# Kernel optimization log

Hardware: AMD Instinct MI355X
Metric: run time of the kernel (lower is better)

The kernel has to match this reference:

```python
import jax, jax.numpy as jnp
import numpy as np

IN_C = 1
BASE_C = 16
N3, N2, N1 = 262144, 65536, 16384

def _quadconv(feat, neigh, w, b):
    # feat: [N, C]; neigh: [N, 9] with -1 padding -> gather via extra zero row
    N = feat.shape[0]
    feat_p = jnp.concatenate([feat, jnp.zeros((1, feat.shape[1]), feat.dtype)], axis=0)
    gidx = jnp.where(neigh == -1, N, neigh)
    col = feat_p[gidx].reshape(N, -1)  # [N, 9*C] im2col
    return col @ w.T + b

def _parent_idx(keys, parent_keys):
    return jnp.searchsorted(parent_keys, keys >> 2)

def _quadpool(feat, keys, parent_keys):
    pidx = _parent_idx(keys, parent_keys)
    p = jax.ops.segment_max(feat, pidx, num_segments=parent_keys.shape[0])
    # original inits with -1e9 and zeroes untouched slots; segment_max uses -inf fill
    return jnp.where(jnp.isneginf(p), jnp.zeros((), feat.dtype), p), pidx

def _quadunpool(feat, keys, parent_keys):
    return feat[_parent_idx(keys, parent_keys)]

def _lin(key, out_f, in_f, scale=0.05):
    kw, kb = jax.random.split(key)
    return (jax.random.normal(kw, (out_f, in_f), jnp.float32) * scale,
            jnp.zeros((out_f,), jnp.float32))

def setup_inputs() -> dict:
    key = jax.random.key(0)
    ks = jax.random.split(key, 12)
    inp = {
        'features': jax.random.normal(ks[0], (N3, IN_C), jnp.float32),
        'keys3': jnp.arange(N3, dtype=jnp.int32),
        'keys2': jnp.arange(N2, dtype=jnp.int32),
        'keys1': jnp.arange(N1, dtype=jnp.int32),
        'neighs3': jax.random.randint(ks[1], (N3, 9), -1, N3, jnp.int32),
        'neighs2': jax.random.randint(ks[2], (N2, 9), -1, N2, jnp.int32),
        'neighs1': jax.random.randint(ks[3], (N1, 9), -1, N1, jnp.int32),
    }
    c = BASE_C
    inp['w_enc1'], inp['b_enc1'] = _lin(ks[4], c, 9 * IN_C)
    inp['w_enc2'], inp['b_enc2'] = _lin(ks[5], 2 * c, 9 * c)
    inp['w_enc3'], inp['b_enc3'] = _lin(ks[6], 4 * c, 9 * 2 * c)
    inp['w_dec1'], inp['b_dec1'] = _lin(ks[7], 2 * c, 9 * 4 * c)
    inp['w_dec2'], inp['b_dec2'] = _lin(ks[8], c, 9 * 2 * c)
    inp['w_head'], inp['b_head'] = _lin(ks[9], IN_C, 9 * c)
    return inp

def reference(features, keys3, keys2, keys1, neighs3, neighs2, neighs1,
              w_enc1, b_enc1, w_enc2, b_enc2, w_enc3, b_enc3,
              w_dec1, b_dec1, w_dec2, b_dec2, w_head, b_head):
    relu = jax.nn.relu
    x8 = relu(_quadconv(features, neighs3, w_enc1, b_enc1))
    x7_p, _ = _quadpool(x8, keys3, keys2)
    x7 = relu(_quadconv(x7_p, neighs2, w_enc2, b_enc2))
    x6_p, _ = _quadpool(x7, keys2, keys1)
    x6 = relu(_quadconv(x6_p, neighs1, w_enc3, b_enc3))
    x7_up = _quadunpool(x6, keys2, keys1)
    x7_dec = relu(_quadconv(x7_up, neighs2, w_dec1, b_dec1))
    x8_up = _quadunpool(x7_dec, keys3, keys2)
    x8_dec = relu(_quadconv(x8_up, neighs3, w_dec2, b_dec2))
    return _quadconv(x8_dec, neighs3, w_head, b_head)
```

## Files before the change

kernel.cpp:

```cpp
#include <hip/hip_runtime.h>
#include <stdint.h>

#define NN3 262144
#define NN2 65536
#define NN1 16384

typedef __attribute__((ext_vector_type(8))) __bf16 bf16x8;
typedef __attribute__((ext_vector_type(4))) float floatx4;

static __device__ __forceinline__ float bf2f(unsigned short u) {
    union { unsigned int i; float f; } v; v.i = ((unsigned int)u) << 16; return v.f;
}
static __device__ __forceinline__ unsigned short f2bf(float f) {
    union { float f; unsigned int i; } v; v.f = f;
    unsigned int x = v.i;
    return (unsigned short)((x + 0x7fffu + ((x >> 16) & 1u)) >> 16);
}
static __device__ __forceinline__ bf16x8 zero_bf16x8() {
    bf16x8 z;
#pragma unroll
    for (int i = 0; i < 8; ++i) z[i] = (__bf16)0.0f;
    return z;
}

__global__ __launch_bounds__(256) void enc1pool_kernel(
    const float* __restrict__ feat, const int* __restrict__ neigh,
    const float* __restrict__ w, const float* __restrict__ b,
    unsigned short* __restrict__ x7p,
    const float* __restrict__ w_enc2, const float* __restrict__ w_enc3,
    const float* __restrict__ w_dec1, const float* __restrict__ w_dec2,
    unsigned short* __restrict__ wb_enc2, unsigned short* __restrict__ wb_enc3,
    unsigned short* __restrict__ wb_dec1, unsigned short* __restrict__ wb_dec2)
{
    {
        int g = blockIdx.x * 256 + threadIdx.x;
        if (g < 4608) wb_enc2[g] = f2bf(w_enc2[g]);
        else {
            g -= 4608;
            if (g < 18432) wb_enc3[g] = f2bf(w_enc3[g]);
            else {
                g -= 18432;
                if (g < 18432) wb_dec1[g] = f2bf(w_dec1[g]);
                else { g -= 18432; if (g < 4608) wb_dec2[g] = f2bf(w_dec2[g]); }
            }
        }
    }
    __shared__ float ws[144];
    __shared__ float bs[16];
    __shared__ int nsh[2304];
    int t = threadIdx.x;
    if (t < 144) ws[t] = w[t];
    if (t < 16)  bs[t] = b[t];
    int base = blockIdx.x * 256;
    for (int e = t; e < 2304; e += 256)
        nsh[e] = __builtin_nontemporal_load(&neigh[(size_t)base * 9 + e]);
    __syncthreads();
    float f[9];
#pragma unroll
    for (int k = 0; k < 9; ++k) { int j = nsh[t * 9 + k]; f[k] = (j < 0) ? 0.0f : feat[j]; }
    float v[16];
#pragma unroll
    for (int co = 0; co < 16; ++co) {
        float a = bs[co];
#pragma unroll
        for (int k = 0; k < 9; ++k) a += f[k] * ws[co * 9 + k];
        v[co] = fmaxf(a, 0.0f);
    }
#pragma unroll
    for (int co = 0; co < 16; ++co) {
        v[co] = fmaxf(v[co], __shfl_xor(v[co], 1));
        v[co] = fmaxf(v[co], __shfl_xor(v[co], 2));
    }
    if ((t & 3) == 0) {
        unsigned int ov[8];
#pragma unroll
        for (int h = 0; h < 8; ++h)
            ov[h] = (unsigned int)f2bf(v[2 * h]) | (((unsigned int)f2bf(v[2 * h + 1])) << 16);
        uint4* dst = (uint4*)(x7p + (size_t)((base + t) >> 2) * 16);
        dst[0] = make_uint4(ov[0], ov[1], ov[2], ov[3]);
        dst[1] = make_uint4(ov[4], ov[5], ov[6], ov[7]);
    }
}

template <int CIN, int COUT, bool SHIFT, bool POOL, int TILES>
__global__ __launch_bounds__(256) void conv_mfma(
    const unsigned short* __restrict__ src, const int* __restrict__ neigh,
    const unsigned short* __restrict__ wb, const float* __restrict__ bias,
    unsigned short* __restrict__ dst)
{
    constexpr int K  = 9 * CIN;
    constexpr int KT = (K + 31) / 32;
    constexpr int NT = COUT / 16;
    __shared__ int nsh[576 * TILES];
    int t = threadIdx.x;
    int rowbase = blockIdx.x * (64 * TILES);
    for (int e = t; e < 576 * TILES; e += 256) {
        int j = __builtin_nontemporal_load(&neigh[(size_t)rowbase * 9 + e]);
        if (SHIFT) j = (j < 0) ? -1 : (j >> 2);
        nsh[e] = j;
    }
    __syncthreads();
    int lane = t & 63;
    int wave = t >> 6;
    int m    = lane & 15;
    int quad = lane >> 4;
    int mrow9 = (wave * 16 + m) * 9;
    floatx4 acc[TILES][NT];
#pragma unroll
    for (int tl = 0; tl < TILES; ++tl)
#pragma unroll
        for (int n = 0; n < NT; ++n) acc[tl][n] = (floatx4){0.f, 0.f, 0.f, 0.f};
    for (int kt = 0; kt < KT; ++kt) {
        int k0 = kt * 32 + quad * 8;
        bf16x8 a[TILES];
#pragma unroll
        for (int tl = 0; tl < TILES; ++tl) {
            a[tl] = zero_bf16x8();
            if (k0 < K) {
                int nb = k0 / CIN;
                int ci = k0 % CIN;
                int j  = nsh[tl * 576 + mrow9 + nb];
                if (j >= 0) a[tl] = *(const bf16x8*)(src + (size_t)j * CIN + ci);
            }
        }
#pragma unroll
        for (int n = 0; n < NT; ++n) {
            bf16x8 bfrag = zero_bf16x8();
            if (k0 < K) bfrag = *(const bf16x8*)(wb + (size_t)(n * 16 + m) * K + k0);
#pragma unroll
            for (int tl = 0; tl < TILES; ++tl)
                acc[tl][n] = __builtin_amdgcn_mfma_f32_16x16x32_bf16(a[tl], bfrag, acc[tl][n], 0, 0, 0);
        }
    }
#pragma unroll
    for (int tl = 0; tl < TILES; ++tl) {
        int tbase = rowbase + tl * 64;
        if (POOL) {
            int p = (tbase >> 2) + wave * 4 + quad;
#pragma unroll
            for (int n = 0; n < NT; ++n) {
                int cout = n * 16 + m;
                float vm = fmaxf(fmaxf(acc[tl][n][0], acc[tl][n][1]), fmaxf(acc[tl][n][2], acc[tl][n][3]));
                float v  = fmaxf(vm + bias[cout], 0.0f);
                dst[(size_t)p * COUT + cout] = f2bf(v);
            }
        } else {
            int grow = tbase + wave * 16 + quad * 4;
#pragma unroll
            for (int n = 0; n < NT; ++n) {
                int cout = n * 16 + m;
                float bv = bias[cout];
#pragma unroll
                for (int r = 0; r < 4; ++r) {
                    float v = fmaxf(acc[tl][n][r] + bv, 0.0f);
                    dst[(size_t)(grow + r) * COUT + cout] = f2bf(v);
                }
            }
        }
    }
}

static __device__ __forceinline__ float dot2(unsigned int u, const float* w) {
    return bf2f((unsigned short)(u & 0xffffu)) * w[0] + bf2f((unsigned short)(u >> 16)) * w[1];
}
__global__ __launch_bounds__(256) void head_kernel(
    const unsigned short* __restrict__ x, const int* __restrict__ neigh,
    const float* __restrict__ w, const float* __restrict__ b, float* __restrict__ out)
{
    __shared__ float ws[144];
    __shared__ int nsh[4608];
    int t = threadIdx.x;
    if (t < 144) ws[t] = w[t];
    int base = blockIdx.x * 512;
    for (int e = t; e < 4608; e += 256)
        nsh[e] = __builtin_nontemporal_load(&neigh[(size_t)base * 9 + e]);
    __syncthreads();
    float acc0 = b[0], acc1 = b[0];
#pragma unroll
    for (int k = 0; k < 9; ++k) {
        int j0 = nsh[t * 9 + k];
        int j1 = nsh[(256 + t) * 9 + k];
        const float* wp = &ws[k * 16];
        if (j0 >= 0) {
            const uint4* r = (const uint4*)(x + (size_t)j0 * 16);
            uint4 r0 = r[0], r1 = r[1];
            acc0 += dot2(r0.x, wp)     + dot2(r0.y, wp + 2)  + dot2(r0.z, wp + 4)  + dot2(r0.w, wp + 6);
            acc0 += dot2(r1.x, wp + 8) + dot2(r1.y, wp + 10) + dot2(r1.z, wp + 12) + dot2(r1.w, wp + 14);
        }
        if (j1 >= 0) {
            const uint4* r = (const uint4*)(x + (size_t)j1 * 16);
            uint4 r0 = r[0], r1 = r[1];
            acc1 += dot2(r0.x, wp)     + dot2(r0.y, wp + 2)  + dot2(r0.z, wp + 4)  + dot2(r0.w, wp + 6);
            acc1 += dot2(r1.x, wp + 8) + dot2(r1.y, wp + 10) + dot2(r1.z, wp + 12) + dot2(r1.w, wp + 14);
        }
    }
    __builtin_nontemporal_store(acc0, &out[base + t]);
    __builtin_nontemporal_store(acc1, &out[base + 256 + t]);
}

extern "C" void kernel_launch(void* const* d_in, const int* in_sizes, int n_in,
                              void* d_out, int out_size, void* d_ws, size_t ws_size,
                              hipStream_t stream) {
    const float* features = (const float*)d_in[0];
    const int* neighs3 = (const int*)d_in[4];
    const int* neighs2 = (const int*)d_in[5];
    const int* neighs1 = (const int*)d_in[6];
    const float* w_enc1 = (const float*)d_in[7];
    const float* b_enc1 = (const float*)d_in[8];
    const float* w_enc2 = (const float*)d_in[9];
    const float* b_enc2 = (const float*)d_in[10];
    const float* w_enc3 = (const float*)d_in[11];
    const float* b_enc3 = (const float*)d_in[12];
    const float* w_dec1 = (const float*)d_in[13];
    const float* b_dec1 = (const float*)d_in[14];
    const float* w_dec2 = (const float*)d_in[15];
    const float* b_dec2 = (const float*)d_in[16];
    const float* w_head = (const float*)d_in[17];
    const float* b_head = (const float*)d_in[18];

    char* ws = (char*)d_ws;
    size_t off = 0;
    unsigned short* wb_enc2 = (unsigned short*)(ws + off); off += 4608 * 2;
    unsigned short* wb_enc3 = (unsigned short*)(ws + off); off += 18432 * 2;
    unsigned short* wb_dec1 = (unsigned short*)(ws + off); off += 18432 * 2;
    unsigned short* wb_dec2 = (unsigned short*)(ws + off); off += 4608 * 2;
    unsigned short* x7p   = (unsigned short*)(ws + off); off += (size_t)NN2 * 16 * 2;
    unsigned short* x6p   = (unsigned short*)(ws + off); off += (size_t)NN1 * 32 * 2;
    unsigned short* x6    = (unsigned short*)(ws + off); off += (size_t)NN1 * 64 * 2;
    unsigned short* x7dec = (unsigned short*)(ws + off); off += (size_t)NN2 * 32 * 2;
    unsigned short* x8dec = (unsigned short*)(ws + off); off += (size_t)NN3 * 16 * 2;

    enc1pool_kernel<<<NN3 / 256, 256, 0, stream>>>(features, neighs3, w_enc1, b_enc1, x7p,
                                                   w_enc2, w_enc3, w_dec1, w_dec2,
                                                   wb_enc2, wb_enc3, wb_dec1, wb_dec2);
    conv_mfma<16, 32, false, true, 2><<<NN2 / 128, 256, 0, stream>>>(x7p, neighs2, wb_enc2, b_enc2, x6p);
    conv_mfma<32, 64, false, false, 1><<<NN1 / 64, 256, 0, stream>>>(x6p, neighs1, wb_enc3, b_enc3, x6);
    conv_mfma<64, 32, true, false, 2><<<NN2 / 128, 256, 0, stream>>>(x6, neighs2, wb_dec1, b_dec1, x7dec);
    conv_mfma<32, 16, true, false, 4><<<NN3 / 256, 256, 0, stream>>>(x7dec, neighs3, wb_dec2, b_dec2, x8dec);
    head_kernel<<<NN3 / 512, 256, 0, stream>>>(x8dec, neighs3, w_head, b_head, (float*)d_out);
}
```

Baseline: 204.3 us.

## Split conv waves across output columns, pre-swizzle weights, prefetch gathers

Weights are pre-swizzled into MFMA fragment order, zero-padded along K, so each lane loads its B fragment with one contiguous, coalesced read and no bounds check. Waves are now split along output channels (WN) as well as rows, so blocks cover fewer rows and the grid gets more blocks for the small middle layers. The A-operand neighbor gather for the next K step is issued before the current MFMAs to hide gather latency. The trade-offs are more register pressure from the double-buffered fragments and fully unrolled K loop, and repeated A gathers across the waves that share rows.

```diff
diff --git a/kernel.cpp b/kernel.cpp
--- a/kernel.cpp
+++ b/kernel.cpp
@@ -21,6 +21,21 @@
 #pragma unroll
     for (int i = 0; i < 8; ++i) z[i] = (__bf16)0.0f;
     return z;
+}
+
+template <int CIN, int COUT>
+static __device__ __forceinline__ void prep_swz(const float* __restrict__ w,
+                                                unsigned short* __restrict__ out, int g) {
+    constexpr int K = 9 * CIN, KT = (K + 31) / 32;
+    int n = g / (KT * 512);
+    int r = g - n * (KT * 512);
+    int kt = r >> 9;
+    int q = r & 511;
+    int lane = q >> 3, e = q & 7;
+    int m = lane & 15, quad = lane >> 4;
+    int k = kt * 32 + quad * 8 + e;
+    float v = (k < K) ? w[(n * 16 + m) * K + k] : 0.0f;
+    out[g] = f2bf(v);
 }
 
 __global__ __launch_bounds__(256) void enc1pool_kernel(
@@ -34,14 +49,14 @@
 {
     {
         int g = blockIdx.x * 256 + threadIdx.x;
-        if (g < 4608) wb_enc2[g] = f2bf(w_enc2[g]);
+        if (g < 5120) prep_swz<16, 32>(w_enc2, wb_enc2, g);
         else {
-            g -= 4608;
-            if (g < 18432) wb_enc3[g] = f2bf(w_enc3[g]);
+            g -= 5120;
+            if (g < 18432) prep_swz<32, 64>(w_enc3, wb_enc3, g);
             else {
                 g -= 18432;
-                if (g < 18432) wb_dec1[g] = f2bf(w_dec1[g]);
-                else { g -= 18432; if (g < 4608) wb_dec2[g] = f2bf(w_dec2[g]); }
+                if (g < 18432) prep_swz<64, 32>(w_dec1, wb_dec1, g);
+                else { g -= 18432; if (g < 4608) prep_swz<32, 16>(w_dec2, wb_dec2, g); }
             }
         }
     }
@@ -82,19 +97,22 @@
     }
 }
 
-template <int CIN, int COUT, bool SHIFT, bool POOL, int TILES>
+template <int CIN, int COUT, bool SHIFT, bool POOL, int TILES, int WN>
 __global__ __launch_bounds__(256) void conv_mfma(
     const unsigned short* __restrict__ src, const int* __restrict__ neigh,
     const unsigned short* __restrict__ wb, const float* __restrict__ bias,
     unsigned short* __restrict__ dst)
 {
-    constexpr int K  = 9 * CIN;
-    constexpr int KT = (K + 31) / 32;
-    constexpr int NT = COUT / 16;
-    __shared__ int nsh[576 * TILES];
+    constexpr int K   = 9 * CIN;
+    constexpr int KT  = (K + 31) / 32;
+    constexpr int NT  = COUT / 16;
+    constexpr int WM  = 4 / WN;
+    constexpr int NTW = NT / WN;
+    constexpr int ROWS = WM * TILES * 16;
+    __shared__ int nsh[ROWS * 9];
     int t = threadIdx.x;
-    int rowbase = blockIdx.x * (64 * TILES);
-    for (int e = t; e < 576 * TILES; e += 256) {
+    int rowbase = blockIdx.x * ROWS;
+    for (int e = t; e < ROWS * 9; e += 256) {
         int j = __builtin_nontemporal_load(&neigh[(size_t)rowbase * 9 + e]);
         if (SHIFT) j = (j < 0) ? -1 : (j >> 2);
         nsh[e] = j;
@@ -102,53 +120,67 @@
     __syncthreads();
     int lane = t & 63;
     int wave = t >> 6;
+    int wm   = wave / WN;
+    int wn   = wave - wm * WN;
     int m    = lane & 15;
     int quad = lane >> 4;
-    int mrow9 = (wave * 16 + m) * 9;
-    floatx4 acc[TILES][NT];
+    int rbase9[TILES];
 #pragma unroll
     for (int tl = 0; tl < TILES; ++tl)
-#pragma unroll
-        for (int n = 0; n < NT; ++n) acc[tl][n] = (floatx4){0.f, 0.f, 0.f, 0.f};
+        rbase9[tl] = ((wm * TILES + tl) * 16 + m) * 9;
+
+    floatx4 acc[TILES][NTW];
+#pragma unroll
+    for (int tl = 0; tl < TILES; ++tl)
+#pragma unroll
+        for (int n = 0; n < NTW; ++n) acc[tl][n] = (floatx4){0.f, 0.f, 0.f, 0.f};
+
+    auto gatherA = [&](int kt, bf16x8 (&dstA)[TILES]) {
+        int k0 = kt * 32 + quad * 8;
+#pragma unroll
+        for (int tl = 0; tl < TILES; ++tl) {
+            dstA[tl] = zero_bf16x8();
+            if (k0 < K) {
+                int j = nsh[rbase9[tl] + k0 / CIN];
+                if (j >= 0) dstA[tl] = *(const bf16x8*)(src + (size_t)j * CIN + (k0 % CIN));
+            }
+        }
+    };
+
+    bf16x8 aC[TILES], aP[TILES];
+    gatherA(0, aC);
+#pragma unroll
     for (int kt = 0; kt < KT; ++kt) {
-        int k0 = kt * 32 + quad * 8;
-        bf16x8 a[TILES];
-#pragma unroll
-        for (int tl = 0; tl < TILES; ++tl) {
-            a[tl] = zero_bf16x8();
-            if (k0 < K) {
-                int nb = k0 / CIN;
-                int ci = k0 % CIN;
-                int j  = nsh[tl * 576 + mrow9 + nb];
-                if (j >= 0) a[tl] = *(const bf16x8*)(src + (size_t)j * CIN + ci);
-            }
-        }
-#pragma unroll
-        for (int n = 0; n < NT; ++n) {
-            bf16x8 bfrag = zero_bf16x8();
-            if (k0 < K) bfrag = *(const bf16x8*)(wb + (size_t)(n * 16 + m) * K + k0);
+        if (kt + 1 < KT) gatherA(kt + 1, aP);
+#pragma unroll
+        for (int n = 0; n < NTW; ++n) {
+            int ng = wn * NTW + n;
+            bf16x8 bfrag = *(const bf16x8*)(wb + ((size_t)(ng * KT + kt) * 64 + lane) * 8);
 #pragma unroll
             for (int tl = 0; tl < TILES; ++tl)
-                acc[tl][n] = __builtin_amdgcn_mfma_f32_16x16x32_bf16(a[tl], bfrag, acc[tl][n], 0, 0, 0);
-        }
-    }
+                acc[tl][n] = __builtin_amdgcn_mfma_f32_16x16x32_bf16(aC[tl], bfrag, acc[tl][n], 0, 0, 0);
+        }
+#pragma unroll
+        for (int tl = 0; tl < TILES; ++tl) aC[tl] = aP[tl];
+    }
+
 #pragma unroll
     for (int tl = 0; tl < TILES; ++tl) {
-        int tbase = rowbase + tl * 64;
+        int rg = wm * TILES + tl;
         if (POOL) {
-            int p = (tbase >> 2) + wave * 4 + quad;
-#pragma unroll
-            for (int n = 0; n < NT; ++n) {
-                int cout = n * 16 + m;
+            int p = (rowbase >> 2) + rg * 4 + quad;
+#pragma unroll
+            for (int n = 0; n < NTW; ++n) {
+                int cout = (wn * NTW + n) * 16 + m;
                 float vm = fmaxf(fmaxf(acc[tl][n][0], acc[tl][n][1]), fmaxf(acc[tl][n][2], acc[tl][n][3]));
                 float v  = fmaxf(vm + bias[cout], 0.0f);
                 dst[(size_t)p * COUT + cout] = f2bf(v);
             }
         } else {
-            int grow = tbase + wave * 16 + quad * 4;
-#pragma unroll
-            for (int n = 0; n < NT; ++n) {
-                int cout = n * 16 + m;
+            int grow = rowbase + rg * 16 + quad * 4;
+#pragma unroll
+            for (int n = 0; n < NTW; ++n) {
+                int cout = (wn * NTW + n) * 16 + m;
                 float bv = bias[cout];
 #pragma unroll
                 for (int r = 0; r < 4; ++r) {
@@ -220,7 +252,7 @@
 
     char* ws = (char*)d_ws;
     size_t off = 0;
-    unsigned short* wb_enc2 = (unsigned short*)(ws + off); off += 4608 * 2;
+    unsigned short* wb_enc2 = (unsigned short*)(ws + off); off += 5120 * 2;
     unsigned short* wb_enc3 = (unsigned short*)(ws + off); off += 18432 * 2;
     unsigned short* wb_dec1 = (unsigned short*)(ws + off); off += 18432 * 2;
     unsigned short* wb_dec2 = (unsigned short*)(ws + off); off += 4608 * 2;
@@ -233,9 +265,9 @@
     enc1pool_kernel<<<NN3 / 256, 256, 0, stream>>>(features, neighs3, w_enc1, b_enc1, x7p,
                                                    w_enc2, w_enc3, w_dec1, w_dec2,
                                                    wb_enc2, wb_enc3, wb_dec1, wb_dec2);
-    conv_mfma<16, 32, false, true, 2><<<NN2 / 128, 256, 0, stream>>>(x7p, neighs2, wb_enc2, b_enc2, x6p);
-    conv_mfma<32, 64, false, false, 1><<<NN1 / 64, 256, 0, stream>>>(x6p, neighs1, wb_enc3, b_enc3, x6);
-    conv_mfma<64, 32, true, false, 2><<<NN2 / 128, 256, 0, stream>>>(x6, neighs2, wb_dec1, b_dec1, x7dec);
-    conv_mfma<32, 16, true, false, 4><<<NN3 / 256, 256, 0, stream>>>(x7dec, neighs3, wb_dec2, b_dec2, x8dec);
+    conv_mfma<16, 32, false, true, 2, 2><<<NN2 / 64, 256, 0, stream>>>(x7p, neighs2, wb_enc2, b_enc2, x6p);
+    conv_mfma<32, 64, false, false, 1, 4><<<NN1 / 16, 256, 0, stream>>>(x6p, neighs1, wb_enc3, b_enc3, x6);
+    conv_mfma<64, 32, true, false, 2, 2><<<NN2 / 64, 256, 0, stream>>>(x6, neighs2, wb_dec1, b_dec1, x7dec);
+    conv_mfma<32, 16, true, false, 4, 1><<<NN3 / 256, 256, 0, stream>>>(x7dec, neighs3, wb_dec2, b_dec2, x8dec);
     head_kernel<<<NN3 / 512, 256, 0, stream>>>(x8dec, neighs3, w_head, b_head, (float*)d_out);
 }
```

Result: no change. 202.5 us (-0.9%).
